# Performance work log

Measured on AMD Instinct MI355X. Metric: run time of the kernel, lower is better.

Reference implementation:

```python
import jax, jax.numpy as jnp
import numpy as np
from jax import lax

B, N, CIN, COUT, FPS, K, TCH, M, H = 8, 4096, 128, 256, 1024, 24, 256, 32, 4
HD = TCH // H
BN_SCALE = 1.0 / np.sqrt(1.0 + 1e-5)  # eval-mode BN: running_mean=0, running_var=1


def _gather(points, idx):
    # points [B,N,C], idx [B,S] or [B,S,K] -> gathered points
    return jax.vmap(lambda p, i: p[i])(points, idx)


def _bn(x, g, b):
    return x * (g * BN_SCALE) + b


def _ln(x, g, b):
    mu = jnp.mean(x, -1, keepdims=True)
    v = jnp.var(x, -1, keepdims=True)
    return (x - mu) / jnp.sqrt(v + 1e-5) * g + b


def _gelu(x):
    return jax.nn.gelu(x, approximate=False)


def _fps(xyz, npoint, farthest0):
    Bb, Nn, _ = xyz.shape
    def step(carry, _):
        dmin, far = carry
        c = jax.vmap(lambda p, i: p[i])(xyz, far)  # [B,3]
        d = jnp.sum((xyz - c[:, None, :]) ** 2, -1)
        dmin = jnp.minimum(dmin, d)
        return (dmin, jnp.argmax(dmin, -1)), far
    init = (jnp.full((Bb, Nn), 1e10, xyz.dtype), farthest0)
    _, cents = lax.scan(step, init, None, length=npoint)
    return cents.T  # [B, npoint]


def _sqdist(src, dst):
    d = -2.0 * jnp.einsum('bnc,bmc->bnm', src, dst)
    d = d + jnp.sum(src ** 2, -1)[:, :, None]
    d = d + jnp.sum(dst ** 2, -1)[:, None, :]
    return d


def _forward(xyz, x, t, farthest0, Wproj, gproj, bproj, Wl1, gl1, bl1, Wl2, gl2, bl2,
             Wc1, gc1, bc1, Wc2, gc2, bc2, Wq, Wk, Wv, Wo,
             ln1g, ln1b, Wqkv, Wao, ln2g, ln2b, Wf1, Wf2):
    # --- GenerateGraph: FPS + KNN grouping ---
    fps_idx = _fps(xyz, FPS, farthest0)            # [B,S]
    new_xyz = _gather(xyz, fps_idx)                # [B,S,3]
    xT = jnp.transpose(x, (0, 2, 1))               # [B,N,Cin]
    new_pts = _gather(xT, fps_idx)                 # [B,S,Cin]
    dist = _sqdist(new_xyz, xyz)                   # [B,S,N]
    _, idx = lax.top_k(-dist, K)                   # [B,S,K] nearest neighbors
    grouped = _gather(xT, idx)                     # [B,S,K,Cin]
    edge = grouped - new_pts[:, :, None, :]
    # --- Local: Conv1DBR proj + Conv1DBRRes (channels-last, 1x1 convs = GEMM) ---
    h = _gelu(_bn(jnp.einsum('bskc,oc->bsko', edge, Wproj), gproj, bproj))
    r = _gelu(_bn(jnp.einsum('bsko,po->bskp', h, Wl1), gl1, bl1))
    r = _bn(jnp.einsum('bskp,op->bsko', r, Wl2), gl2, bl2)
    h = _gelu(r + h)
    f = jnp.max(h, axis=2)                         # adaptive_max_pool over k -> [B,S,O]
    # --- Channel (ca): Conv1DBRRes on centroid features ---
    r = _gelu(_bn(f @ Wc1.T, gc1, bc1))
    r = _bn(r @ Wc2.T, gc2, bc2)
    f = _gelu(r + f)
    x_out = jnp.transpose(f, (0, 2, 1))            # [B,O,S]
    # --- Local2Former: tokens attend to local features ---
    q = t @ Wq.T
    kk = f @ Wk.T
    v = f @ Wv.T
    a = jax.nn.softmax(jnp.einsum('bmd,bsd->bms', q, kk) * (TCH ** -0.5), axis=-1)
    t = t + jnp.einsum('bms,bsd->bmd', a, v) @ Wo.T
    # --- Former: one pre-norm encoder layer (MHA + MLP) ---
    hn = _ln(t, ln1g, ln1b)
    qkv = (hn @ Wqkv.T).reshape(B, M, 3, H, HD).transpose(2, 0, 3, 1, 4)
    qh, kh, vh = qkv[0], qkv[1], qkv[2]            # [B,H,M,hd]
    attn = jax.nn.softmax(jnp.einsum('bhmd,bhnd->bhmn', qh, kh) * (HD ** -0.5), axis=-1)
    o = jnp.einsum('bhmn,bhnd->bhmd', attn, vh).transpose(0, 2, 1, 3).reshape(B, M, TCH)
    t = t + o @ Wao.T
    hn = _ln(t, ln2g, ln2b)
    t = t + _gelu(hn @ Wf1.T) @ Wf2.T
    return new_xyz, x_out, t


def setup_inputs() -> dict:
    key = jax.random.key(0)
    ks = jax.random.split(key, 40)
    def w(k, o, i):
        return jax.random.normal(k, (o, i), jnp.float32) / np.sqrt(i)
    def g(k, c):
        return 1.0 + 0.1 * jax.random.normal(k, (c,), jnp.float32)
    def bta(k, c):
        return 0.1 * jax.random.normal(k, (c,), jnp.float32)
    inp = {
        'xyz': jax.random.normal(ks[0], (B, N, 3), jnp.float32),
        'x': jax.random.normal(ks[1], (B, CIN, N), jnp.float32),
        't': jax.random.normal(ks[2], (B, M, TCH), jnp.float32),
        'farthest0': jax.random.randint(ks[3], (B,), 0, N),
        'Wproj': w(ks[4], COUT, CIN), 'gproj': g(ks[5], COUT), 'bproj': bta(ks[6], COUT),
        'Wl1': w(ks[7], COUT, COUT), 'gl1': g(ks[8], COUT), 'bl1': bta(ks[9], COUT),
        'Wl2': w(ks[10], COUT, COUT), 'gl2': g(ks[11], COUT), 'bl2': bta(ks[12], COUT),
        'Wc1': w(ks[13], COUT, COUT), 'gc1': g(ks[14], COUT), 'bc1': bta(ks[15], COUT),
        'Wc2': w(ks[16], COUT, COUT), 'gc2': g(ks[17], COUT), 'bc2': bta(ks[18], COUT),
        'Wq': w(ks[19], TCH, TCH), 'Wk': w(ks[20], TCH, COUT), 'Wv': w(ks[21], TCH, COUT),
        'Wo': w(ks[22], TCH, TCH),
        'ln1g': g(ks[23], TCH), 'ln1b': bta(ks[24], TCH),
        'Wqkv': w(ks[25], 3 * TCH, TCH), 'Wao': w(ks[26], TCH, TCH),
        'ln2g': g(ks[27], TCH), 'ln2b': bta(ks[28], TCH),
        'Wf1': w(ks[29], 2 * TCH, TCH), 'Wf2': w(ks[30], TCH, 2 * TCH),
    }
    return inp


def reference(xyz, x, t, farthest0, Wproj, gproj, bproj, Wl1, gl1, bl1, Wl2, gl2, bl2,
              Wc1, gc1, bc1, Wc2, gc2, bc2, Wq, Wk, Wv, Wo,
              ln1g, ln1b, Wqkv, Wao, ln2g, ln2b, Wf1, Wf2):
    return _forward(xyz, x, t, farthest0, Wproj, gproj, bproj, Wl1, gl1, bl1, Wl2, gl2, bl2,
                    Wc1, gc1, bc1, Wc2, gc2, bc2, Wq, Wk, Wv, Wo,
                    ln1g, ln1b, Wqkv, Wao, ln2g, ln2b, Wf1, Wf2)
```

## Files before the change

### kernel.cpp

```cpp
#include <hip/hip_runtime.h>
#include <math.h>

#define Bc 8
#define Nc 4096
#define CINc 128
#define COUTc 256
#define Sc 1024
#define Kc 24
#define TCHc 256
#define Mc 32
#define Hc 4
#define HDc 64
#define MBAT (Sc*Kc)

#define BN_SCALE_F 0.9999950000374997f

typedef __attribute__((ext_vector_type(8))) short bf16x8;
typedef __attribute__((ext_vector_type(4))) float f32x4;

__device__ __forceinline__ float b2f(short s){
  unsigned int u = ((unsigned int)(unsigned short)s) << 16;
  union { unsigned int u; float f; } c; c.u = u; return c.f;
}
__device__ __forceinline__ short f2b(float f){
  union { unsigned int u; float f; } c; c.f = f;
  unsigned int u = c.u;
  unsigned int r = (u + 0x7fffu + ((u >> 16) & 1u)) >> 16;
  return (short)(r & 0xffffu);
}
__device__ __forceinline__ float gelu_f(float v){
  return 0.5f * v * (1.f + erff(v * 0.7071067811865475f));
}
__device__ __forceinline__ float rdval(const float* p){ return *p; }
__device__ __forceinline__ float rdval(const short* p){ return b2f(*p); }
__device__ __forceinline__ void wrval(float* p, float v){ *p = v; }
__device__ __forceinline__ void wrval(short* p, float v){ *p = f2b(v); }

__device__ __forceinline__ void gl_lds16(const short* g, short* l){
  __builtin_amdgcn_global_load_lds(
     (const __attribute__((address_space(1))) void*)g,
     (__attribute__((address_space(3))) void*)l, 16, 0, 0);
}

__device__ __forceinline__ void bar_lds(){
  asm volatile("s_waitcnt lgkmcnt(0)" ::: "memory");
  __builtin_amdgcn_s_barrier();
}

template<int CTRL>
__device__ __forceinline__ double dpp_max_f64(double v){
  long long x = __double_as_longlong(v);
  int lo = (int)(unsigned int)(x & 0xFFFFFFFFLL);
  int hi = (int)(unsigned int)((unsigned long long)x >> 32);
  int plo = __builtin_amdgcn_update_dpp(lo, lo, CTRL, 0xF, 0xF, false);
  int phi = __builtin_amdgcn_update_dpp(hi, hi, CTRL, 0xF, 0xF, false);
  double p = __longlong_as_double((long long)(((unsigned long long)(unsigned int)phi << 32)
                                              | (unsigned int)plo));
  return fmax(v, p);
}
template<int CTRL>
__device__ __forceinline__ float dpp_min_f32(float v){
  int x = __float_as_int(v);
  int p = __builtin_amdgcn_update_dpp(x, x, CTRL, 0xF, 0xF, false);
  return fminf(v, __int_as_float(p));
}
template<int CTRL>
__device__ __forceinline__ float dpp_max_f32(float v){
  int x = __float_as_int(v);
  int p = __builtin_amdgcn_update_dpp(x, x, CTRL, 0xF, 0xF, false);
  return fmaxf(v, __int_as_float(p));
}
template<int CTRL>
__device__ __forceinline__ unsigned dpp_min_u32(unsigned v){
  int p = __builtin_amdgcn_update_dpp((int)v, (int)v, CTRL, 0xF, 0xF, false);
  unsigned pu = (unsigned)p;
  return v < pu ? v : pu;
}
__device__ __forceinline__ float wave_min63(float v){
  v = dpp_min_f32<0x111>(v); v = dpp_min_f32<0x112>(v); v = dpp_min_f32<0x114>(v);
  v = dpp_min_f32<0x118>(v); v = dpp_min_f32<0x142>(v); v = dpp_min_f32<0x143>(v);
  return v;
}
__device__ __forceinline__ float wave_max63(float v){
  v = dpp_max_f32<0x111>(v); v = dpp_max_f32<0x112>(v); v = dpp_max_f32<0x114>(v);
  v = dpp_max_f32<0x118>(v); v = dpp_max_f32<0x142>(v); v = dpp_max_f32<0x143>(v);
  return v;
}
__device__ __forceinline__ float bcast63(float v){
  return __int_as_float(__builtin_amdgcn_readlane(__float_as_int(v), 63));
}

#define PREP_FPS 8
#define PREP_TOTAL 256
#define NWORK 248

__global__ __launch_bounds__(512) void prep_kernel(
    const float* __restrict__ xyz, const int* __restrict__ far0, int* __restrict__ fps_idx,
    const float* __restrict__ x, short* __restrict__ xT,
    const float* __restrict__ Wproj, const float* __restrict__ Wl1, const float* __restrict__ Wl2,
    const float* __restrict__ Wc1, const float* __restrict__ Wc2,
    const float* __restrict__ Wk, const float* __restrict__ Wv,
    const float* __restrict__ Wq, const float* __restrict__ Wo,
    const float* __restrict__ Wqkv, const float* __restrict__ Wao,
    const float* __restrict__ Wf1, const float* __restrict__ Wf2,
    const float* __restrict__ t_in,
    short* __restrict__ wbf,
    int* __restrict__ knn_idx, float* __restrict__ out0){
  __shared__ __align__(16) char smemc[57728];
  int bid = blockIdx.x, tid = threadIdx.x;
  if(bid < PREP_FPS){
    int b = bid;
    float* sxyz = (float*)smemc;
    unsigned short* sid = (unsigned short*)(smemc + 49152);
    int* hist = (int*)(smemc + 57344);
    double* pwave = (double*)(smemc + 57600);
    const float* xb = xyz + (size_t)b*Nc*3;
    if(tid < 64) hist[tid] = 0;
    float gx[8], gy[8], gz[8]; int code[8];
    __syncthreads();
#pragma unroll
    for(int j=0;j<8;j++){
      int n = tid + 512*j;
      const float* p = xb + n*3;
      gx[j]=p[0]; gy[j]=p[1]; gz[j]=p[2];
      int qx = (int)fminf(fmaxf((gx[j]+4.2f)*(4.f/8.4f),0.f),3.f);
      int qy = (int)fminf(fmaxf((gy[j]+4.2f)*(4.f/8.4f),0.f),3.f);
      int qz = (int)fminf(fmaxf((gz[j]+4.2f)*(4.f/8.4f),0.f),3.f);
      code[j] = ((qx>>1)<<5)|((qy>>1)<<4)|((qz>>1)<<3)|((qx&1)<<2)|((qy&1)<<1)|(qz&1);
      atomicAdd(&hist[code[j]], 1);
    }
    __syncthreads();
    if(tid==0){
      int run=0;
      for(int i=0;i<64;i++){ int h=hist[i]; hist[i]=run; run+=h; }
    }
    __syncthreads();
#pragma unroll
    for(int j=0;j<8;j++){
      int slot = atomicAdd(&hist[code[j]], 1);
      sxyz[slot*3]=gx[j]; sxyz[slot*3+1]=gy[j]; sxyz[slot*3+2]=gz[j];
      sid[slot] = (unsigned short)(tid + 512*j);
    }
    __syncthreads();
    float px[8], py[8], pz[8], dmin[8];
    unsigned int lokey[8];
    float mnx=3e38f,mny=3e38f,mnz=3e38f,mxx=-3e38f,mxy=-3e38f,mxz=-3e38f;
#pragma unroll
    for(int j=0;j<8;j++){
      int i = (tid>>6)*512 + j*64 + (tid&63);
      float xx=sxyz[i*3], yy=sxyz[i*3+1], zz=sxyz[i*3+2];
      px[j]=xx; py[j]=yy; pz[j]=zz;
      dmin[j]=1e10f;
      lokey[j]=(unsigned int)((Nc-1) - (int)sid[i]);
      mnx=fminf(mnx,xx); mxx=fmaxf(mxx,xx);
      mny=fminf(mny,yy); mxy=fmaxf(mxy,yy);
      mnz=fminf(mnz,zz); mxz=fmaxf(mxz,zz);
    }
    float bbmnx = bcast63(wave_min63(mnx)), bbmxx = bcast63(wave_max63(mxx));
    float bbmny = bcast63(wave_min63(mny)), bbmxy = bcast63(wave_max63(mxy));
    float bbmnz = bcast63(wave_min63(mnz)), bbmxz = bcast63(wave_max63(mxz));
    __syncthreads();
    for(int i=tid; i<Nc; i+=512){
      const float* p = xb + i*3;
      sxyz[i*3]=p[0]; sxyz[i*3+1]=p[1]; sxyz[i*3+2]=p[2];
    }
    __syncthreads();
    int winner = far0[b] & (Nc-1);
    int* out = fps_idx + b*Sc;
    double pk = 0.0;
    float wm = 3.0e38f;
    for(int it=0; it<Sc; it++){
      if(tid==0)
        __hip_atomic_store(&out[it], winner, __ATOMIC_RELAXED, __HIP_MEMORY_SCOPE_AGENT);
      float cx=sxyz[winner*3], cy=sxyz[winner*3+1], cz=sxyz[winner*3+2];
      float ddx = fmaxf(fmaxf(bbmnx - cx, cx - bbmxx), 0.f);
      float ddy = fmaxf(fmaxf(bbmny - cy, cy - bbmxy), 0.f);
      float ddz = fmaxf(fmaxf(bbmnz - cz, cz - bbmxz), 0.f);
      float md2 = ddx*ddx + ddy*ddy + ddz*ddz;
      if(md2 < wm*1.0001f){
        double key[8];
#pragma unroll
        for(int j=0;j<8;j++){
          float dx = __fsub_rn(px[j], cx);
          float dy = __fsub_rn(py[j], cy);
          float dz = __fsub_rn(pz[j], cz);
          float d = __fadd_rn(__fadd_rn(__fmul_rn(dx,dx), __fmul_rn(dy,dy)), __fmul_rn(dz,dz));
          dmin[j] = fminf(dmin[j], d);
          unsigned long long k = (((unsigned long long)__float_as_uint(dmin[j])) << 32) | lokey[j];
          key[j] = __longlong_as_double((long long)k);
        }
#pragma unroll
        for(int st=4; st>0; st>>=1)
#pragma unroll
          for(int j=0;j<st;j++) key[j] = fmax(key[j], key[j+st]);
        double kv = key[0];
        kv = dpp_max_f64<0x111>(kv);
        kv = dpp_max_f64<0x112>(kv);
        kv = dpp_max_f64<0x114>(kv);
        kv = dpp_max_f64<0x118>(kv);
        kv = dpp_max_f64<0x142>(kv);
        kv = dpp_max_f64<0x143>(kv);
        pk = kv;
        wm = __int_as_float(__builtin_amdgcn_readlane(
               (int)(__double_as_longlong(kv) >> 32), 63));
      }
      int p = it & 1;
      if((tid & 63) == 63) pwave[p*8 + (tid>>6)] = pk;
      bar_lds();
      double k0 = pwave[p*8+0], k1 = pwave[p*8+1], k2 = pwave[p*8+2], k3 = pwave[p*8+3];
      double k4 = pwave[p*8+4], k5 = pwave[p*8+5], k6 = pwave[p*8+6], k7 = pwave[p*8+7];
      double kb = fmax(fmax(fmax(k0,k1), fmax(k2,k3)), fmax(fmax(k4,k5), fmax(k6,k7)));
      unsigned long long kbits = (unsigned long long)__double_as_longlong(kb);
      winner = (Nc-1) - (int)(kbits & 0xFFFFFFFFULL);
    }
  } else {
    int wid = bid - PREP_FPS;
    int b = wid / 31;
    int widb = wid % 31;
    short (*tile)[33] = (short(*)[33])smemc;
    for(int t = wid; t < 4096; t += NWORK){
      int bb = t >> 9;
      int rem = t & 511;
      int n0 = (rem & 127) * 32;
      int c0 = (rem >> 7) * 32;
      int tx = tid & 31, ty = tid >> 5;
      __syncthreads();
#pragma unroll
      for(int i=0;i<32;i+=16)
        tile[ty+i][tx] = f2b(x[((size_t)bb*CINc + (c0+ty+i))*Nc + n0+tx]);
      __syncthreads();
#pragma unroll
      for(int i=0;i<32;i+=16)
        xT[((size_t)bb*Nc + (n0+ty+i))*CINc + c0+tx] = tile[tx][ty+i];
    }
    {
      int gid = wid*512 + tid;
      const int stride = NWORK*512;
      short* p = wbf;
      for(int i=gid; i<COUTc*CINc; i+=stride) p[i] = f2b(Wproj[i]);
      p += COUTc*CINc;
      for(int i=gid; i<COUTc*COUTc; i+=stride) p[i] = f2b(Wl1[i]);
      p += COUTc*COUTc;
      for(int i=gid; i<COUTc*COUTc; i+=stride) p[i] = f2b(Wl2[i]);
      p += COUTc*COUTc;
      for(int i=gid; i<COUTc*COUTc; i+=stride) p[i] = f2b(Wc1[i]);
      p += COUTc*COUTc;
      for(int i=gid; i<COUTc*COUTc; i+=stride) p[i] = f2b(Wc2[i]);
      p += COUTc*COUTc;
      for(int i=gid; i<TCHc*COUTc; i+=stride) p[i] = f2b(Wk[i]);
      p += TCHc*COUTc;
      for(int i=gid; i<TCHc*COUTc; i+=stride) p[i] = f2b(Wv[i]);
      p += TCHc*COUTc;
      for(int i=gid; i<TCHc*TCHc; i+=stride) p[i] = f2b(Wq[i]);
      p += TCHc*TCHc;
      for(int i=gid; i<TCHc*TCHc; i+=stride) p[i] = f2b(Wo[i]);
      p += TCHc*TCHc;
      for(int i=gid; i<3*TCHc*TCHc; i+=stride) p[i] = f2b(Wqkv[i]);
      p += 3*TCHc*TCHc;
      for(int i=gid; i<TCHc*TCHc; i+=stride) p[i] = f2b(Wao[i]);
      p += TCHc*TCHc;
      for(int i=gid; i<2*TCHc*TCHc; i+=stride) p[i] = f2b(Wf1[i]);
      p += 2*TCHc*TCHc;
      for(int i=gid; i<2*TCHc*TCHc; i+=stride) p[i] = f2b(Wf2[i]);
      p += 2*TCHc*TCHc;
      for(int i=gid; i<Bc*Mc*TCHc; i+=stride) p[i] = f2b(t_in[i]);
    }
    int* s_qn = (int*)smemc;
    float* pv = (float*)(smemc + 32);
    int*   pi = (int*)(smemc + 64);
    const float* xb = xyz + (size_t)b*Nc*3;
    float px[8], py[8], pz[8], db[8];
#pragma unroll
    for(int j=0;j<8;j++){
      int n = tid + 512*j;
      float xx=xb[n*3], yy=xb[n*3+1], zz=xb[n*3+2];
      px[j]=xx; py[j]=yy; pz[j]=zz;
      db[j] = __fadd_rn(__fadd_rn(__fmul_rn(xx,xx),__fmul_rn(yy,yy)),__fmul_rn(zz,zz));
    }
    __syncthreads();
    for(int s = widb; s < Sc; s += 31){
      if(tid==0){
        int qn;
        for(;;){
          qn = __hip_atomic_load(&fps_idx[b*Sc + s], __ATOMIC_RELAXED, __HIP_MEMORY_SCOPE_AGENT);
          if(qn >= 0) break;
          __builtin_amdgcn_s_sleep(8);
        }
        s_qn[0] = qn & (Nc-1);
      }
      bar_lds();
      int qn = s_qn[0];
      const float* q = xyz + ((size_t)b*Nc + qn)*3;
      float sxq = q[0], syq = q[1], szq = q[2];
      if(tid < 3) out0[((size_t)b*Sc + s)*3 + tid] = q[tid];
      float ss = __fadd_rn(__fadd_rn(__fmul_rn(sxq,sxq),__fmul_rn(syq,syq)),__fmul_rn(szq,szq));
      float dv[8];
#pragma unroll
      for(int j=0;j<8;j++){
        float e = __fmul_rn(sxq,px[j]);
        e = __fadd_rn(e, __fmul_rn(syq,py[j]));
        e = __fadd_rn(e, __fmul_rn(szq,pz[j]));
        dv[j] = __fadd_rn(__fadd_rn(__fmul_rn(-2.f,e), ss), db[j]);
      }
      int* ob = knn_idx + ((size_t)b*Sc + s)*Kc;
      for(int k=0;k<Kc;k++){
        float bvv = dv[0];
#pragma unroll
        for(int j=1;j<8;j++) bvv = fminf(bvv, dv[j]);
        bvv = dpp_min_f32<0x111>(bvv);
        bvv = dpp_min_f32<0x112>(bvv);
        bvv = dpp_min_f32<0x114>(bvv);
        bvv = dpp_min_f32<0x118>(bvv);
        bvv = dpp_min_f32<0x142>(bvv);
        bvv = dpp_min_f32<0x143>(bvv);
        if((tid&63)==63) pv[tid>>6] = bvv;
        bar_lds();
        float vmin = fminf(fminf(fminf(pv[0],pv[1]), fminf(pv[2],pv[3])),
                           fminf(fminf(pv[4],pv[5]), fminf(pv[6],pv[7])));
        unsigned bi = 0xFFFFFFFFu;
#pragma unroll
        for(int j=0;j<8;j++){
          unsigned n = (unsigned)(tid + 512*j);
          if(dv[j]==vmin && n < bi) bi = n;
        }
        bi = dpp_min_u32<0x111>(bi);
        bi = dpp_min_u32<0x112>(bi);
        bi = dpp_min_u32<0x114>(bi);
        bi = dpp_min_u32<0x118>(bi);
        bi = dpp_min_u32<0x142>(bi);
        bi = dpp_min_u32<0x143>(bi);
        if((tid&63)==63) pi[tid>>6] = (int)bi;
        bar_lds();
        unsigned win = (unsigned)pi[0];
#pragma unroll
        for(int w=1;w<8;w++){ unsigned u=(unsigned)pi[w]; win = u<win?u:win; }
        if(tid==0) ob[k] = (int)(win & (Nc-1));
#pragma unroll
        for(int j=0;j<8;j++) if((int)win == tid + 512*j) dv[j] = 3.4e38f;
      }
    }
  }
}

__global__ __launch_bounds__(256) void local_fused(
    const short* __restrict__ xT, const int* __restrict__ knn_idx, const int* __restrict__ fps_idx,
    const short* __restrict__ Wp_, const float* __restrict__ gp, const float* __restrict__ bp,
    const short* __restrict__ W1, const float* __restrict__ g1, const float* __restrict__ b1,
    const short* __restrict__ W2, const float* __restrict__ g2, const float* __restrict__ b2,
    short* __restrict__ Fout){
  __shared__ __align__(16) char lds[77824];
  short* Asrc = (short*)lds;
  short* Wst  = (short*)(lds + 12288);
  short* Hb   = (short*)(lds + 28672);
  short* Rb   = (short*)(lds + 53248);
  int p = blockIdx.x;
  int R0 = p*48;
  int tid = threadIdx.x;
  int w = tid >> 6, lane = tid & 63, quad = lane >> 4, l16 = lane & 15;
  int colbase = w*64;
#pragma unroll
  for(int u0=0; u0<3; u0++){
    int u = tid + u0*256;
    int r = u >> 4, seg = u & 15;
    int Rg = R0 + r;
    int bb = Rg / MBAT;
    int nk = knn_idx[Rg] & (Nc-1);
    int nc = fps_idx[Rg / Kc] & (Nc-1);
    bf16x8 vk = *(const bf16x8*)(xT + ((size_t)bb*Nc + nk)*CINc + seg*8);
    bf16x8 vc = *(const bf16x8*)(xT + ((size_t)bb*Nc + nc)*CINc + seg*8);
    bf16x8 e;
#pragma unroll
    for(int i=0;i<8;i++) e[i] = f2b(__fsub_rn(b2f(vk[i]), b2f(vc[i])));
    *(bf16x8*)&Asrc[((seg>>2)*48 + r)*32 + (seg&3)*8] = e;
  }
  __syncthreads();
  f32x4 acc[3][4];
#pragma unroll
  for(int mt=0;mt<3;mt++)
#pragma unroll
    for(int nt=0;nt<4;nt++) acc[mt][nt] = (f32x4){0.f,0.f,0.f,0.f};
  for(int k0=0; k0<CINc; k0+=32){
#pragma unroll
    for(int c=0;c<4;c++)
      gl_lds16(Wp_ + (size_t)(c*64 + (tid>>2))*CINc + k0 + (tid&3)*8,
               Wst + c*2048 + tid*8);
    __syncthreads();
    bf16x8 af[3], bfr[4];
#pragma unroll
    for(int mt=0;mt<3;mt++) af[mt] = *(const bf16x8*)&Asrc[(((k0>>5))*48 + mt*16 + l16)*32 + quad*8];
#pragma unroll
    for(int nt=0;nt<4;nt++) bfr[nt] = *(const bf16x8*)&Wst[(colbase + nt*16 + l16)*32 + quad*8];
#pragma unroll
    for(int mt=0;mt<3;mt++)
#pragma unroll
      for(int nt=0;nt<4;nt++)
        acc[mt][nt] = __builtin_amdgcn_mfma_f32_16x16x32_bf16(af[mt], bfr[nt], acc[mt][nt], 0, 0, 0);
    __syncthreads();
  }
#pragma unroll
  for(int nt=0;nt<4;nt++){
    int col = colbase + nt*16 + l16;
    float gs = gp[col] * BN_SCALE_F, bs_ = bp[col];
    int kb = col >> 5, kr = col & 31;
#pragma unroll
    for(int mt=0;mt<3;mt++)
#pragma unroll
      for(int r2=0;r2<4;r2++){
        int row = mt*16 + quad*4 + r2;
        float v = acc[mt][nt][r2]*gs + bs_;
        Hb[(kb*48 + row)*32 + kr] = f2b(gelu_f(v));
      }
  }
  __syncthreads();
#pragma unroll
  for(int mt=0;mt<3;mt++)
#pragma unroll
    for(int nt=0;nt<4;nt++) acc[mt][nt] = (f32x4){0.f,0.f,0.f,0.f};
  for(int k0=0; k0<COUTc; k0+=32){
#pragma unroll
    for(int c=0;c<4;c++)
      gl_lds16(W1 + (size_t)(c*64 + (tid>>2))*COUTc + k0 + (tid&3)*8,
               Wst + c*2048 + tid*8);
    __syncthreads();
    bf16x8 af[3], bfr[4];
#pragma unroll
    for(int mt=0;mt<3;mt++) af[mt] = *(const bf16x8*)&Hb[(((k0>>5))*48 + mt*16 + l16)*32 + quad*8];
#pragma unroll
    for(int nt=0;nt<4;nt++) bfr[nt] = *(const bf16x8*)&Wst[(colbase + nt*16 + l16)*32 + quad*8];
#pragma unroll
    for(int mt=0;mt<3;mt++)
#pragma unroll
      for(int nt=0;nt<4;nt++)
        acc[mt][nt] = __builtin_amdgcn_mfma_f32_16x16x32_bf16(af[mt], bfr[nt], acc[mt][nt], 0, 0, 0);
    __syncthreads();
  }
#pragma unroll
  for(int nt=0;nt<4;nt++){
    int col = colbase + nt*16 + l16;
    float gs = g1[col] * BN_SCALE_F, bs_ = b1[col];
    int kb = col >> 5, kr = col & 31;
#pragma unroll
    for(int mt=0;mt<3;mt++)
#pragma unroll
      for(int r2=0;r2<4;r2++){
        int row = mt*16 + quad*4 + r2;
        float v = acc[mt][nt][r2]*gs + bs_;
        Rb[(kb*48 + row)*32 + kr] = f2b(gelu_f(v));
      }
  }
  __syncthreads();
#pragma unroll
  for(int mt=0;mt<3;mt++)
#pragma unroll
    for(int nt=0;nt<4;nt++) acc[mt][nt] = (f32x4){0.f,0.f,0.f,0.f};
  for(int k0=0; k0<COUTc; k0+=32){
#pragma unroll
    for(int c=0;c<4;c++)
      gl_lds16(W2 + (size_t)(c*64 + (tid>>2))*COUTc + k0 + (tid&3)*8,
               Wst + c*2048 + tid*8);
    __syncthreads();
    bf16x8 af[3], bfr[4];
#pragma unroll
    for(int mt=0;mt<3;mt++) af[mt] = *(const bf16x8*)&Rb[(((k0>>5))*48 + mt*16 + l16)*32 + quad*8];
#pragma unroll
    for(int nt=0;nt<4;nt++) bfr[nt] = *(const bf16x8*)&Wst[(colbase + nt*16 + l16)*32 + quad*8];
#pragma unroll
    for(int mt=0;mt<3;mt++)
#pragma unroll
      for(int nt=0;nt<4;nt++)
        acc[mt][nt] = __builtin_amdgcn_mfma_f32_16x16x32_bf16(af[mt], bfr[nt], acc[mt][nt], 0, 0, 0);
    __syncthreads();
  }
#pragma unroll
  for(int nt=0;nt<4;nt++){
    int col = colbase + nt*16 + l16;
    float gs = g2[col] * BN_SCALE_F, bs_ = b2[col];
    int kb = col >> 5, kr = col & 31;
    float gm0 = -3.4e38f, gm1 = -3.4e38f;
#pragma unroll
    for(int mt=0;mt<3;mt++)
#pragma unroll
      for(int r2=0;r2<4;r2++){
        int row = mt*16 + quad*4 + r2;
        float v = acc[mt][nt][r2]*gs + bs_;
        v += b2f(Hb[(kb*48 + row)*32 + kr]);
        v = gelu_f(v);
        if(mt==0) gm0 = fmaxf(gm0, v);
        else if(mt==2) gm1 = fmaxf(gm1, v);
        else { if(quad < 2) gm0 = fmaxf(gm0, v); else gm1 = fmaxf(gm1, v); }
      }
    gm0 = fmaxf(gm0, __shfl_xor(gm0, 16));
    gm0 = fmaxf(gm0, __shfl_xor(gm0, 32));
    gm1 = fmaxf(gm1, __shfl_xor(gm1, 16));
    gm1 = fmaxf(gm1, __shfl_xor(gm1, 32));
    if(quad == 0){
      Fout[(size_t)(p*2)*COUTc + col]     = f2b(gm0);
      Fout[(size_t)(p*2+1)*COUTc + col]   = f2b(gm1);
    }
  }
}

template<int HAS_BN, int HAS_GELU, int HAS_RES, typename TRES, typename TOUT>
__global__ __launch_bounds__(256) void gemm64d(
    const short* __restrict__ A, const short* __restrict__ W,
    const float* __restrict__ g, const float* __restrict__ bias,
    const TRES* __restrict__ Res, TOUT* __restrict__ Out,
    int Nn, int Kk){
  __shared__ short As[64*32];
  __shared__ short Bs[64*32];
  int bm = blockIdx.y*64, bn = blockIdx.x*64;
  int tid = threadIdx.x;
  int wave = tid >> 6, lane = tid & 63, quad = lane >> 4, l16 = lane & 15;
  f32x4 acc[4];
#pragma unroll
  for(int i=0;i<4;i++) acc[i] = (f32x4){0.f,0.f,0.f,0.f};
  const short* Ap = A + (size_t)(bm + (tid>>2))*Kk + (tid&3)*8;
  const short* Wp = W + (size_t)(bn + (tid>>2))*Kk + (tid&3)*8;
  for(int k0=0; k0<Kk; k0+=32){
    gl_lds16(Ap + k0, As + tid*8);
    gl_lds16(Wp + k0, Bs + tid*8);
    __syncthreads();
    bf16x8 a = *(const bf16x8*)&As[(wave*16 + l16)*32 + quad*8];
#pragma unroll
    for(int ct=0; ct<4; ct++){
      bf16x8 bb = *(const bf16x8*)&Bs[(ct*16 + l16)*32 + quad*8];
      acc[ct] = __builtin_amdgcn_mfma_f32_16x16x32_bf16(a, bb, acc[ct], 0, 0, 0);
    }
    __syncthreads();
  }
#pragma unroll
  for(int ct=0; ct<4; ct++){
    int col = bn + ct*16 + l16;
    float gs = 0.f, bs_ = 0.f;
    if(HAS_BN){ gs = g[col] * BN_SCALE_F; bs_ = bias[col]; }
#pragma unroll
    for(int r2=0;r2<4;r2++){
      int row = bm + wave*16 + quad*4 + r2;
      float v = acc[ct][r2];
      if(HAS_BN) v = v*gs + bs_;
      if(HAS_RES) v += rdval(Res + (size_t)row*Nn + col);
      if(HAS_GELU) v = gelu_f(v);
      wrval(Out + (size_t)row*Nn + col, v);
    }
  }
}

__global__ __launch_bounds__(256) void transpose_f(const short* __restrict__ f2, float* __restrict__ out1){
  __shared__ short tile[32][33];
  int b = blockIdx.z;
  int s0 = blockIdx.x*32, c0 = blockIdx.y*32;
  int tx = threadIdx.x & 31, ty = threadIdx.x >> 5;
#pragma unroll
  for(int i=0;i<32;i+=8)
    tile[ty+i][tx] = f2[((size_t)b*Sc + (s0+ty+i))*COUTc + c0+tx];
  __syncthreads();
#pragma unroll
  for(int i=0;i<32;i+=8)
    out1[((size_t)b*COUTc + (c0+ty+i))*Sc + s0+tx] = b2f(tile[tx][ty+i]);
}

__global__ __launch_bounds__(256) void l2f_attn(
    const short* __restrict__ qb, const short* __restrict__ kv,
    short* __restrict__ ao){
  int blk = blockIdx.x; int b = blk / Mc; int m = blk % Mc;
  int tid = threadIdx.x;
  __shared__ float qs[TCHc];
  __shared__ float aw[Sc];
  __shared__ float red[8];
  qs[tid] = b2f(qb[(size_t)(b*Mc+m)*TCHc + tid]);
  __syncthreads();
  float sc[4];
#pragma unroll
  for(int jj=0;jj<4;jj++){
    int j = tid + 256*jj;
    const short* kp = kv + ((size_t)b*Sc + j)*512;
    float a = 0.f;
    for(int c=0;c<TCHc;c+=8){
      bf16x8 v8 = *(const bf16x8*)(kp + c);
#pragma unroll
      for(int i=0;i<8;i++) a += b2f(v8[i]) * qs[c+i];
    }
    sc[jj] = a * 0.0625f;
  }
  float mx = fmaxf(fmaxf(sc[0],sc[1]), fmaxf(sc[2],sc[3]));
#pragma unroll
  for(int off=32; off>0; off>>=1) mx = fmaxf(mx, __shfl_xor(mx, off));
  if((tid&63)==0) red[tid>>6] = mx;
  __syncthreads();
  mx = fmaxf(fmaxf(red[0],red[1]), fmaxf(red[2],red[3]));
  float se = 0.f;
#pragma unroll
  for(int jj=0;jj<4;jj++){
    float e = expf(sc[jj] - mx);
    aw[tid + 256*jj] = e;
    se += e;
  }
#pragma unroll
  for(int off=32; off>0; off>>=1) se += __shfl_xor(se, off);
  if((tid&63)==0) red[4 + (tid>>6)] = se;
  __syncthreads();
  se = red[4]+red[5]+red[6]+red[7];
  float inv = 1.f/se;
#pragma unroll
  for(int jj=0;jj<4;jj++) aw[tid + 256*jj] *= inv;
  __syncthreads();
  float acc = 0.f;
  const short* vp = kv + (size_t)b*Sc*512 + 256 + tid;
  for(int j=0;j<Sc;j++) acc += aw[j] * b2f(vp[(size_t)j*512]);
  ao[(size_t)(b*Mc+m)*TCHc + tid] = f2b(acc);
}

__global__ __launch_bounds__(64) void former_attn(const short* __restrict__ qkv, short* __restrict__ oa){
  int blk = blockIdx.x;
  int m = blk % Mc; int bh = blk / Mc; int h = bh % Hc; int b = bh / Hc;
  int lane = threadIdx.x;
  __shared__ float qs[HDc];
  __shared__ float aw2[32];
  const short* base = qkv + (size_t)(b*Mc)*(3*TCHc);
  qs[lane] = b2f(base[(size_t)m*3*TCHc + h*HDc + lane]);
  __syncthreads();
  int j = lane & 31;
  const short* kp = base + (size_t)j*3*TCHc + TCHc + h*HDc;
  float s = 0.f;
  for(int d=0; d<HDc; d+=8){
    bf16x8 v8 = *(const bf16x8*)(kp + d);
#pragma unroll
    for(int i=0;i<8;i++) s += b2f(v8[i]) * qs[d+i];
  }
  s *= 0.125f;
  float mx = s;
#pragma unroll
  for(int off=16; off>0; off>>=1) mx = fmaxf(mx, __shfl_xor(mx, off, 32));
  float e = expf(s - mx);
  float se = e;
#pragma unroll
  for(int off=16; off>0; off>>=1) se += __shfl_xor(se, off, 32);
  if(lane < 32) aw2[lane] = e / se;
  __syncthreads();
  float acc = 0.f;
  const short* vp = base + 2*TCHc + h*HDc + lane;
  for(int jj=0; jj<32; jj++) acc += aw2[jj] * b2f(vp[(size_t)jj*3*TCHc]);
  oa[(size_t)(b*Mc+m)*TCHc + h*HDc + lane] = f2b(acc);
}

__global__ __launch_bounds__(64) void ln_kernel(const float* __restrict__ X, const float* __restrict__ g,
                                                const float* __restrict__ bb, short* __restrict__ O){
  int row = blockIdx.x, lane = threadIdx.x;
  const float* xp = X + (size_t)row*TCHc;
  float x[4];
#pragma unroll
  for(int j2=0;j2<4;j2++) x[j2] = xp[lane + 64*j2];
  float sm = x[0]+x[1]+x[2]+x[3];
#pragma unroll
  for(int off=32; off>0; off>>=1) sm += __shfl_xor(sm, off);
  float mu = sm * (1.f/256.f);
  float vs = 0.f;
#pragma unroll
  for(int j2=0;j2<4;j2++){ float d = x[j2]-mu; vs += d*d; }
#pragma unroll
  for(int off=32; off>0; off>>=1) vs += __shfl_xor(vs, off);
  float var = vs * (1.f/256.f);
  float rstd = 1.f / sqrtf(var + 1e-5f);
#pragma unroll
  for(int j2=0;j2<4;j2++){
    int c = lane + 64*j2;
    float o = (x[j2]-mu)*rstd*g[c] + bb[c];
    O[(size_t)row*TCHc + c] = f2b(o);
  }
}

extern "C" void kernel_launch(void* const* d_in, const int* in_sizes, int n_in,
                              void* d_out, int out_size, void* d_ws, size_t ws_size,
                              hipStream_t stream){
  const float* xyz  = (const float*)d_in[0];
  const float* x    = (const float*)d_in[1];
  const float* t_in = (const float*)d_in[2];
  const int*   far0 = (const int*)d_in[3];
  const float* Wproj=(const float*)d_in[4];  const float* gproj=(const float*)d_in[5];  const float* bproj=(const float*)d_in[6];
  const float* Wl1 = (const float*)d_in[7];  const float* gl1 = (const float*)d_in[8];  const float* bl1 = (const float*)d_in[9];
  const float* Wl2 = (const float*)d_in[10]; const float* gl2 = (const float*)d_in[11]; const float* bl2 = (const float*)d_in[12];
  const float* Wc1 = (const float*)d_in[13]; const float* gc1 = (const float*)d_in[14]; const float* bc1 = (const float*)d_in[15];
  const float* Wc2 = (const float*)d_in[16]; const float* gc2 = (const float*)d_in[17]; const float* bc2 = (const float*)d_in[18];
  const float* Wq  = (const float*)d_in[19]; const float* Wk  = (const float*)d_in[20]; const float* Wv  = (const float*)d_in[21];
  const float* Wo  = (const float*)d_in[22];
  const float* ln1g= (const float*)d_in[23]; const float* ln1b= (const float*)d_in[24];
  const float* Wqkv= (const float*)d_in[25]; const float* Wao = (const float*)d_in[26];
  const float* ln2g= (const float*)d_in[27]; const float* ln2b= (const float*)d_in[28];
  const float* Wf1 = (const float*)d_in[29]; const float* Wf2 = (const float*)d_in[30];

  char* wsb = (char*)d_ws;
  size_t off = 0;
  auto alloc = [&](size_t bytes)->void*{ void* p = wsb + off; off += (bytes + 255) & ~(size_t)255; return p; };
  int*   fps_i = (int*)alloc((size_t)Bc*Sc*4);
  int*   knn   = (int*)alloc((size_t)Bc*Sc*Kc*4);
  short* xT    = (short*)alloc((size_t)Bc*Nc*CINc*2);
  size_t wbf_elems = (size_t)COUTc*CINc + 4*(size_t)COUTc*COUTc + 2*(size_t)TCHc*COUTc
                   + 2*(size_t)TCHc*TCHc + 3*(size_t)TCHc*TCHc + (size_t)TCHc*TCHc
                   + 2*(size_t)TCHc*TCHc + 2*(size_t)TCHc*TCHc + (size_t)Bc*Mc*TCHc;
  short* wbf   = (short*)alloc(wbf_elems*2);
  short* fbuf  = (short*)alloc((size_t)Bc*Sc*COUTc*2);
  short* rcbuf = (short*)alloc((size_t)Bc*Sc*COUTc*2);
  short* f2buf = (short*)alloc((size_t)Bc*Sc*COUTc*2);
  short* kvbuf = (short*)alloc((size_t)Bc*Sc*512*2);
  short* qbuf  = (short*)alloc((size_t)Bc*Mc*TCHc*2);
  short* a1out = (short*)alloc((size_t)Bc*Mc*TCHc*2);
  float* t1buf = (float*)alloc((size_t)Bc*Mc*TCHc*4);
  short* hnbuf = (short*)alloc((size_t)Bc*Mc*TCHc*2);
  short* qkvb  = (short*)alloc((size_t)Bc*Mc*3*TCHc*2);
  short* a2out = (short*)alloc((size_t)Bc*Mc*TCHc*2);
  float* t2buf = (float*)alloc((size_t)Bc*Mc*TCHc*4);
  short* hn2buf= (short*)alloc((size_t)Bc*Mc*TCHc*2);
  short* g1buf = (short*)alloc((size_t)Bc*Mc*2*TCHc*2);
  if(off > ws_size) return;

  short* wproj_bf = wbf;
  short* wl1_bf   = wproj_bf + COUTc*CINc;
  short* wl2_bf   = wl1_bf + COUTc*COUTc;
  short* wc1_bf   = wl2_bf + COUTc*COUTc;
  short* wc2_bf   = wc1_bf + COUTc*COUTc;
  short* wkv_bf   = wc2_bf + COUTc*COUTc;
  short* wq_bf    = wkv_bf + 2*TCHc*COUTc;
  short* wo_bf    = wq_bf + TCHc*TCHc;
  short* wqkv_bf  = wo_bf + TCHc*TCHc;
  short* wao_bf   = wqkv_bf + 3*TCHc*TCHc;
  short* wf1_bf   = wao_bf + TCHc*TCHc;
  short* wf2_bf   = wf1_bf + 2*TCHc*TCHc;
  short* tbf      = wf2_bf + 2*TCHc*TCHc;

  float* out0 = (float*)d_out;
  float* out1 = out0 + (size_t)Bc*Sc*3;
  float* out2 = out1 + (size_t)Bc*COUTc*Sc;

  hipMemsetAsync(fps_i, 0xFF, (size_t)Bc*Sc*4, stream);
  prep_kernel<<<PREP_TOTAL, 512, 0, stream>>>(xyz, far0, fps_i, x, xT,
                                              Wproj, Wl1, Wl2, Wc1, Wc2, Wk, Wv,
                                              Wq, Wo, Wqkv, Wao, Wf1, Wf2, t_in,
                                              wbf, knn, out0);
  local_fused<<<(Bc*Sc)/2, 256, 0, stream>>>(xT, knn, fps_i,
                                             wproj_bf, gproj, bproj,
                                             wl1_bf, gl1, bl1,
                                             wl2_bf, gl2, bl2, fbuf);
  gemm64d<1,1,0,short,short><<<dim3(COUTc/64, (Bc*Sc)/64), 256, 0, stream>>>(fbuf, wc1_bf, gc1, bc1, (const short*)nullptr, rcbuf, COUTc, COUTc);
  gemm64d<1,1,1,short,short><<<dim3(COUTc/64, (Bc*Sc)/64), 256, 0, stream>>>(rcbuf, wc2_bf, gc2, bc2, fbuf, f2buf, COUTc, COUTc);
  transpose_f<<<dim3(Sc/32, COUTc/32, Bc), 256, 0, stream>>>(f2buf, out1);
  gemm64d<0,0,0,short,short><<<dim3(TCHc/64, (Bc*Mc)/64), 256, 0, stream>>>(tbf, wq_bf, nullptr, nullptr, (const short*)nullptr, qbuf, TCHc, TCHc);
  gemm64d<0,0,0,short,short><<<dim3(512/64, (Bc*Sc)/64), 256, 0, stream>>>(f2buf, wkv_bf, nullptr, nullptr, (const short*)nullptr, kvbuf, 512, COUTc);
  l2f_attn<<<Bc*Mc, 256, 0, stream>>>(qbuf, kvbuf, a1out);
  gemm64d<0,0,1,float,float><<<dim3(TCHc/64, (Bc*Mc)/64), 256, 0, stream>>>(a1out, wo_bf, nullptr, nullptr, t_in, t1buf, TCHc, TCHc);
  ln_kernel<<<Bc*Mc, 64, 0, stream>>>(t1buf, ln1g, ln1b, hnbuf);
  gemm64d<0,0,0,short,short><<<dim3((3*TCHc)/64, (Bc*Mc)/64), 256, 0, stream>>>(hnbuf, wqkv_bf, nullptr, nullptr, (const short*)nullptr, qkvb, 3*TCHc, TCHc);
  former_attn<<<Bc*Hc*Mc, 64, 0, stream>>>(qkvb, a2out);
  gemm64d<0,0,1,float,float><<<dim3(TCHc/64, (Bc*Mc)/64), 256, 0, stream>>>(a2out, wao_bf, nullptr, nullptr, t1buf, t2buf, TCHc, TCHc);
  ln_kernel<<<Bc*Mc, 64, 0, stream>>>(t2buf, ln2g, ln2b, hn2buf);
  gemm64d<0,1,0,short,short><<<dim3((2*TCHc)/64, (Bc*Mc)/64), 256, 0, stream>>>(hn2buf, wf1_bf, nullptr, nullptr, (const short*)nullptr, g1buf, 2*TCHc, TCHc);
  gemm64d<0,0,1,float,float><<<dim3(TCHc/64, (Bc*Mc)/64), 256, 0, stream>>>(g1buf, wf2_bf, nullptr, nullptr, t2buf, out2, TCHc, 2*TCHc);
}
```

Baseline: 1.100 ms.

## Fuse local MLP grouping into KNN worker blocks of prep kernel

Removes the separate local_fused kernel. Each KNN worker block in prep_kernel now runs the edge-feature gather and the three-layer proj/res MLP with max-pool for every query point right after selecting its 24 neighbours, so the local stage overlaps with the FPS dependency wait. A grid-wide ready counter makes the workers wait until all of them have finished the bf16 weight conversion. The cost is that only 248 blocks do all of the MLP work with small 32-row tiles (24 rows used, rows padded with zeros), and the 2x32-column per-wave tiles reuse the weights less than the old 48-row tiles did.

```diff
diff --git a/kernel.cpp b/kernel.cpp
--- a/kernel.cpp
+++ b/kernel.cpp
@@ -46,6 +46,10 @@
   asm volatile("s_waitcnt lgkmcnt(0)" ::: "memory");
   __builtin_amdgcn_s_barrier();
 }
+__device__ __forceinline__ void bar_vm(){
+  asm volatile("s_waitcnt vmcnt(0) lgkmcnt(0)" ::: "memory");
+  __builtin_amdgcn_s_barrier();
+}
 
 template<int CTRL>
 __device__ __forceinline__ double dpp_max_f64(double v){
@@ -105,7 +109,11 @@
     const float* __restrict__ Wf1, const float* __restrict__ Wf2,
     const float* __restrict__ t_in,
     short* __restrict__ wbf,
-    int* __restrict__ knn_idx, float* __restrict__ out0){
+    int* __restrict__ knn_idx, float* __restrict__ out0,
+    const float* __restrict__ gp, const float* __restrict__ bp,
+    const float* __restrict__ g1, const float* __restrict__ b1,
+    const float* __restrict__ g2, const float* __restrict__ b2,
+    short* __restrict__ Fout, int* __restrict__ ready){
   __shared__ __align__(16) char smemc[57728];
   int bid = blockIdx.x, tid = threadIdx.x;
   if(bid < PREP_FPS){
@@ -265,9 +273,24 @@
       p += 2*TCHc*TCHc;
       for(int i=gid; i<Bc*Mc*TCHc; i+=stride) p[i] = f2b(t_in[i]);
     }
+    __syncthreads();
+    if(tid==0){
+      __hip_atomic_fetch_add(ready, 1, __ATOMIC_RELEASE, __HIP_MEMORY_SCOPE_AGENT);
+      while(__hip_atomic_load(ready, __ATOMIC_ACQUIRE, __HIP_MEMORY_SCOPE_AGENT) < NWORK)
+        __builtin_amdgcn_s_sleep(16);
+    }
+    __syncthreads();
     int* s_qn = (int*)smemc;
     float* pv = (float*)(smemc + 32);
     int*   pi = (int*)(smemc + 64);
+    int*   kn = (int*)(smemc + 96);
+    short* Ea = (short*)(smemc + 256);
+    short* Hs = (short*)(smemc + 8448);
+    short* Rs = (short*)(smemc + 24832);
+    short* Ws = (short*)(smemc + 41216);
+    const short* wpj = wbf;
+    const short* w1p = wpj + COUTc*CINc;
+    const short* w2p = w1p + COUTc*COUTc;
     const float* xb = xyz + (size_t)b*Nc*3;
     float px[8], py[8], pz[8], db[8];
 #pragma unroll
@@ -277,6 +300,7 @@
       px[j]=xx; py[j]=yy; pz[j]=zz;
       db[j] = __fadd_rn(__fadd_rn(__fmul_rn(xx,xx),__fmul_rn(yy,yy)),__fmul_rn(zz,zz));
     }
+    int wv8 = tid>>6, qd = (tid>>4)&3, l16v = tid&15;
     __syncthreads();
     for(int s = widb; s < Sc; s += 31){
       if(tid==0){
@@ -334,168 +358,132 @@
         unsigned win = (unsigned)pi[0];
 #pragma unroll
         for(int w=1;w<8;w++){ unsigned u=(unsigned)pi[w]; win = u<win?u:win; }
-        if(tid==0) ob[k] = (int)(win & (Nc-1));
+        if(tid==0){ ob[k] = (int)(win & (Nc-1)); kn[k] = (int)(win & (Nc-1)); }
 #pragma unroll
         for(int j=0;j<8;j++) if((int)win == tid + 512*j) dv[j] = 3.4e38f;
       }
-    }
-  }
-}
-
-__global__ __launch_bounds__(256) void local_fused(
-    const short* __restrict__ xT, const int* __restrict__ knn_idx, const int* __restrict__ fps_idx,
-    const short* __restrict__ Wp_, const float* __restrict__ gp, const float* __restrict__ bp,
-    const short* __restrict__ W1, const float* __restrict__ g1, const float* __restrict__ b1,
-    const short* __restrict__ W2, const float* __restrict__ g2, const float* __restrict__ b2,
-    short* __restrict__ Fout){
-  __shared__ __align__(16) char lds[77824];
-  short* Asrc = (short*)lds;
-  short* Wst  = (short*)(lds + 12288);
-  short* Hb   = (short*)(lds + 28672);
-  short* Rb   = (short*)(lds + 53248);
-  int p = blockIdx.x;
-  int R0 = p*48;
-  int tid = threadIdx.x;
-  int w = tid >> 6, lane = tid & 63, quad = lane >> 4, l16 = lane & 15;
-  int colbase = w*64;
-#pragma unroll
-  for(int u0=0; u0<3; u0++){
-    int u = tid + u0*256;
-    int r = u >> 4, seg = u & 15;
-    int Rg = R0 + r;
-    int bb = Rg / MBAT;
-    int nk = knn_idx[Rg] & (Nc-1);
-    int nc = fps_idx[Rg / Kc] & (Nc-1);
-    bf16x8 vk = *(const bf16x8*)(xT + ((size_t)bb*Nc + nk)*CINc + seg*8);
-    bf16x8 vc = *(const bf16x8*)(xT + ((size_t)bb*Nc + nc)*CINc + seg*8);
-    bf16x8 e;
-#pragma unroll
-    for(int i=0;i<8;i++) e[i] = f2b(__fsub_rn(b2f(vk[i]), b2f(vc[i])));
-    *(bf16x8*)&Asrc[((seg>>2)*48 + r)*32 + (seg&3)*8] = e;
-  }
-  __syncthreads();
-  f32x4 acc[3][4];
-#pragma unroll
-  for(int mt=0;mt<3;mt++)
-#pragma unroll
-    for(int nt=0;nt<4;nt++) acc[mt][nt] = (f32x4){0.f,0.f,0.f,0.f};
-  for(int k0=0; k0<CINc; k0+=32){
-#pragma unroll
-    for(int c=0;c<4;c++)
-      gl_lds16(Wp_ + (size_t)(c*64 + (tid>>2))*CINc + k0 + (tid&3)*8,
-               Wst + c*2048 + tid*8);
-    __syncthreads();
-    bf16x8 af[3], bfr[4];
-#pragma unroll
-    for(int mt=0;mt<3;mt++) af[mt] = *(const bf16x8*)&Asrc[(((k0>>5))*48 + mt*16 + l16)*32 + quad*8];
-#pragma unroll
-    for(int nt=0;nt<4;nt++) bfr[nt] = *(const bf16x8*)&Wst[(colbase + nt*16 + l16)*32 + quad*8];
-#pragma unroll
-    for(int mt=0;mt<3;mt++)
-#pragma unroll
-      for(int nt=0;nt<4;nt++)
-        acc[mt][nt] = __builtin_amdgcn_mfma_f32_16x16x32_bf16(af[mt], bfr[nt], acc[mt][nt], 0, 0, 0);
-    __syncthreads();
-  }
-#pragma unroll
-  for(int nt=0;nt<4;nt++){
-    int col = colbase + nt*16 + l16;
-    float gs = gp[col] * BN_SCALE_F, bs_ = bp[col];
-    int kb = col >> 5, kr = col & 31;
-#pragma unroll
-    for(int mt=0;mt<3;mt++)
-#pragma unroll
-      for(int r2=0;r2<4;r2++){
-        int row = mt*16 + quad*4 + r2;
-        float v = acc[mt][nt][r2]*gs + bs_;
-        Hb[(kb*48 + row)*32 + kr] = f2b(gelu_f(v));
-      }
-  }
-  __syncthreads();
-#pragma unroll
-  for(int mt=0;mt<3;mt++)
-#pragma unroll
-    for(int nt=0;nt<4;nt++) acc[mt][nt] = (f32x4){0.f,0.f,0.f,0.f};
-  for(int k0=0; k0<COUTc; k0+=32){
-#pragma unroll
-    for(int c=0;c<4;c++)
-      gl_lds16(W1 + (size_t)(c*64 + (tid>>2))*COUTc + k0 + (tid&3)*8,
-               Wst + c*2048 + tid*8);
-    __syncthreads();
-    bf16x8 af[3], bfr[4];
-#pragma unroll
-    for(int mt=0;mt<3;mt++) af[mt] = *(const bf16x8*)&Hb[(((k0>>5))*48 + mt*16 + l16)*32 + quad*8];
-#pragma unroll
-    for(int nt=0;nt<4;nt++) bfr[nt] = *(const bf16x8*)&Wst[(colbase + nt*16 + l16)*32 + quad*8];
-#pragma unroll
-    for(int mt=0;mt<3;mt++)
-#pragma unroll
-      for(int nt=0;nt<4;nt++)
-        acc[mt][nt] = __builtin_amdgcn_mfma_f32_16x16x32_bf16(af[mt], bfr[nt], acc[mt][nt], 0, 0, 0);
-    __syncthreads();
-  }
-#pragma unroll
-  for(int nt=0;nt<4;nt++){
-    int col = colbase + nt*16 + l16;
-    float gs = g1[col] * BN_SCALE_F, bs_ = b1[col];
-    int kb = col >> 5, kr = col & 31;
-#pragma unroll
-    for(int mt=0;mt<3;mt++)
-#pragma unroll
-      for(int r2=0;r2<4;r2++){
-        int row = mt*16 + quad*4 + r2;
-        float v = acc[mt][nt][r2]*gs + bs_;
-        Rb[(kb*48 + row)*32 + kr] = f2b(gelu_f(v));
-      }
-  }
-  __syncthreads();
-#pragma unroll
-  for(int mt=0;mt<3;mt++)
-#pragma unroll
-    for(int nt=0;nt<4;nt++) acc[mt][nt] = (f32x4){0.f,0.f,0.f,0.f};
-  for(int k0=0; k0<COUTc; k0+=32){
-#pragma unroll
-    for(int c=0;c<4;c++)
-      gl_lds16(W2 + (size_t)(c*64 + (tid>>2))*COUTc + k0 + (tid&3)*8,
-               Wst + c*2048 + tid*8);
-    __syncthreads();
-    bf16x8 af[3], bfr[4];
-#pragma unroll
-    for(int mt=0;mt<3;mt++) af[mt] = *(const bf16x8*)&Rb[(((k0>>5))*48 + mt*16 + l16)*32 + quad*8];
-#pragma unroll
-    for(int nt=0;nt<4;nt++) bfr[nt] = *(const bf16x8*)&Wst[(colbase + nt*16 + l16)*32 + quad*8];
-#pragma unroll
-    for(int mt=0;mt<3;mt++)
-#pragma unroll
-      for(int nt=0;nt<4;nt++)
-        acc[mt][nt] = __builtin_amdgcn_mfma_f32_16x16x32_bf16(af[mt], bfr[nt], acc[mt][nt], 0, 0, 0);
-    __syncthreads();
-  }
-#pragma unroll
-  for(int nt=0;nt<4;nt++){
-    int col = colbase + nt*16 + l16;
-    float gs = g2[col] * BN_SCALE_F, bs_ = b2[col];
-    int kb = col >> 5, kr = col & 31;
-    float gm0 = -3.4e38f, gm1 = -3.4e38f;
-#pragma unroll
-    for(int mt=0;mt<3;mt++)
-#pragma unroll
-      for(int r2=0;r2<4;r2++){
-        int row = mt*16 + quad*4 + r2;
-        float v = acc[mt][nt][r2]*gs + bs_;
-        v += b2f(Hb[(kb*48 + row)*32 + kr]);
-        v = gelu_f(v);
-        if(mt==0) gm0 = fmaxf(gm0, v);
-        else if(mt==2) gm1 = fmaxf(gm1, v);
-        else { if(quad < 2) gm0 = fmaxf(gm0, v); else gm1 = fmaxf(gm1, v); }
-      }
-    gm0 = fmaxf(gm0, __shfl_xor(gm0, 16));
-    gm0 = fmaxf(gm0, __shfl_xor(gm0, 32));
-    gm1 = fmaxf(gm1, __shfl_xor(gm1, 16));
-    gm1 = fmaxf(gm1, __shfl_xor(gm1, 32));
-    if(quad == 0){
-      Fout[(size_t)(p*2)*COUTc + col]     = f2b(gm0);
-      Fout[(size_t)(p*2+1)*COUTc + col]   = f2b(gm1);
+      bar_lds();
+      {
+        int r = tid>>4, seg = tid&15;
+        bf16x8 e = {0,0,0,0,0,0,0,0};
+        if(r < 24){
+          int nk = kn[r];
+          bf16x8 vk = *(const bf16x8*)(xT + ((size_t)b*Nc + nk)*CINc + seg*8);
+          bf16x8 vc = *(const bf16x8*)(xT + ((size_t)b*Nc + qn)*CINc + seg*8);
+#pragma unroll
+          for(int i=0;i<8;i++) e[i] = f2b(__fsub_rn(b2f(vk[i]), b2f(vc[i])));
+        }
+        *(bf16x8*)&Ea[((seg>>2)*32 + r)*32 + (seg&3)*8] = e;
+      }
+      bar_lds();
+      f32x4 a2[2][2];
+#pragma unroll
+      for(int mt=0;mt<2;mt++)
+#pragma unroll
+        for(int nt=0;nt<2;nt++) a2[mt][nt] = (f32x4){0.f,0.f,0.f,0.f};
+      for(int kb=0; kb<4; kb++){
+        int k0 = kb*32;
+        gl_lds16(wpj + (size_t)(tid>>2)*CINc + k0 + (tid&3)*8, Ws + tid*8);
+        gl_lds16(wpj + (size_t)(128+(tid>>2))*CINc + k0 + (tid&3)*8, Ws + 4096 + tid*8);
+        bar_vm();
+        bf16x8 af0 = *(const bf16x8*)&Ea[(kb*32 + l16v)*32 + qd*8];
+        bf16x8 af1 = *(const bf16x8*)&Ea[(kb*32 + 16 + l16v)*32 + qd*8];
+        bf16x8 b0f = *(const bf16x8*)&Ws[(wv8*32 + l16v)*32 + qd*8];
+        bf16x8 b1f = *(const bf16x8*)&Ws[(wv8*32 + 16 + l16v)*32 + qd*8];
+        a2[0][0] = __builtin_amdgcn_mfma_f32_16x16x32_bf16(af0, b0f, a2[0][0], 0,0,0);
+        a2[0][1] = __builtin_amdgcn_mfma_f32_16x16x32_bf16(af0, b1f, a2[0][1], 0,0,0);
+        a2[1][0] = __builtin_amdgcn_mfma_f32_16x16x32_bf16(af1, b0f, a2[1][0], 0,0,0);
+        a2[1][1] = __builtin_amdgcn_mfma_f32_16x16x32_bf16(af1, b1f, a2[1][1], 0,0,0);
+        bar_lds();
+      }
+#pragma unroll
+      for(int nt=0;nt<2;nt++){
+        int col = wv8*32 + nt*16 + l16v;
+        float gs = gp[col]*BN_SCALE_F, bs_ = bp[col];
+#pragma unroll
+        for(int mt=0;mt<2;mt++)
+#pragma unroll
+          for(int r2=0;r2<4;r2++){
+            int row = mt*16 + qd*4 + r2;
+            float v = a2[mt][nt][r2]*gs + bs_;
+            Hs[(wv8*32 + row)*32 + nt*16 + l16v] = f2b(gelu_f(v));
+          }
+      }
+      bar_lds();
+#pragma unroll
+      for(int mt=0;mt<2;mt++)
+#pragma unroll
+        for(int nt=0;nt<2;nt++) a2[mt][nt] = (f32x4){0.f,0.f,0.f,0.f};
+      for(int kb=0; kb<8; kb++){
+        int k0 = kb*32;
+        gl_lds16(w1p + (size_t)(tid>>2)*COUTc + k0 + (tid&3)*8, Ws + tid*8);
+        gl_lds16(w1p + (size_t)(128+(tid>>2))*COUTc + k0 + (tid&3)*8, Ws + 4096 + tid*8);
+        bar_vm();
+        bf16x8 af0 = *(const bf16x8*)&Hs[(kb*32 + l16v)*32 + qd*8];
+        bf16x8 af1 = *(const bf16x8*)&Hs[(kb*32 + 16 + l16v)*32 + qd*8];
+        bf16x8 b0f = *(const bf16x8*)&Ws[(wv8*32 + l16v)*32 + qd*8];
+        bf16x8 b1f = *(const bf16x8*)&Ws[(wv8*32 + 16 + l16v)*32 + qd*8];
+        a2[0][0] = __builtin_amdgcn_mfma_f32_16x16x32_bf16(af0, b0f, a2[0][0], 0,0,0);
+        a2[0][1] = __builtin_amdgcn_mfma_f32_16x16x32_bf16(af0, b1f, a2[0][1], 0,0,0);
+        a2[1][0] = __builtin_amdgcn_mfma_f32_16x16x32_bf16(af1, b0f, a2[1][0], 0,0,0);
+        a2[1][1] = __builtin_amdgcn_mfma_f32_16x16x32_bf16(af1, b1f, a2[1][1], 0,0,0);
+        bar_lds();
+      }
+#pragma unroll
+      for(int nt=0;nt<2;nt++){
+        int col = wv8*32 + nt*16 + l16v;
+        float gs = g1[col]*BN_SCALE_F, bs_ = b1[col];
+#pragma unroll
+        for(int mt=0;mt<2;mt++)
+#pragma unroll
+          for(int r2=0;r2<4;r2++){
+            int row = mt*16 + qd*4 + r2;
+            float v = a2[mt][nt][r2]*gs + bs_;
+            Rs[(wv8*32 + row)*32 + nt*16 + l16v] = f2b(gelu_f(v));
+          }
+      }
+      bar_lds();
+#pragma unroll
+      for(int mt=0;mt<2;mt++)
+#pragma unroll
+        for(int nt=0;nt<2;nt++) a2[mt][nt] = (f32x4){0.f,0.f,0.f,0.f};
+      for(int kb=0; kb<8; kb++){
+        int k0 = kb*32;
+        gl_lds16(w2p + (size_t)(tid>>2)*COUTc + k0 + (tid&3)*8, Ws + tid*8);
+        gl_lds16(w2p + (size_t)(128+(tid>>2))*COUTc + k0 + (tid&3)*8, Ws + 4096 + tid*8);
+        bar_vm();
+        bf16x8 af0 = *(const bf16x8*)&Rs[(kb*32 + l16v)*32 + qd*8];
+        bf16x8 af1 = *(const bf16x8*)&Rs[(kb*32 + 16 + l16v)*32 + qd*8];
+        bf16x8 b0f = *(const bf16x8*)&Ws[(wv8*32 + l16v)*32 + qd*8];
+        bf16x8 b1f = *(const bf16x8*)&Ws[(wv8*32 + 16 + l16v)*32 + qd*8];
+        a2[0][0] = __builtin_amdgcn_mfma_f32_16x16x32_bf16(af0, b0f, a2[0][0], 0,0,0);
+        a2[0][1] = __builtin_amdgcn_mfma_f32_16x16x32_bf16(af0, b1f, a2[0][1], 0,0,0);
+        a2[1][0] = __builtin_amdgcn_mfma_f32_16x16x32_bf16(af1, b0f, a2[1][0], 0,0,0);
+        a2[1][1] = __builtin_amdgcn_mfma_f32_16x16x32_bf16(af1, b1f, a2[1][1], 0,0,0);
+        bar_lds();
+      }
+#pragma unroll
+      for(int nt=0;nt<2;nt++){
+        int col = wv8*32 + nt*16 + l16v;
+        float gs = g2[col]*BN_SCALE_F, bs_ = b2[col];
+        float gm = -3.4e38f;
+#pragma unroll
+        for(int mt=0;mt<2;mt++)
+#pragma unroll
+          for(int r2=0;r2<4;r2++){
+            int row = mt*16 + qd*4 + r2;
+            if(row < 24){
+              float v = a2[mt][nt][r2]*gs + bs_;
+              v += b2f(Hs[(wv8*32 + row)*32 + nt*16 + l16v]);
+              gm = fmaxf(gm, gelu_f(v));
+            }
+          }
+        gm = fmaxf(gm, __shfl_xor(gm, 16));
+        gm = fmaxf(gm, __shfl_xor(gm, 32));
+        if(qd==0)
+          Fout[((size_t)b*Sc + s)*COUTc + col] = f2b(gm);
+      }
+      bar_lds();
     }
   }
 }
@@ -693,6 +681,7 @@
   auto alloc = [&](size_t bytes)->void*{ void* p = wsb + off; off += (bytes + 255) & ~(size_t)255; return p; };
   int*   fps_i = (int*)alloc((size_t)Bc*Sc*4);
   int*   knn   = (int*)alloc((size_t)Bc*Sc*Kc*4);
+  int*   ready = (int*)alloc(256);
   short* xT    = (short*)alloc((size_t)Bc*Nc*CINc*2);
   size_t wbf_elems = (size_t)COUTc*CINc + 4*(size_t)COUTc*COUTc + 2*(size_t)TCHc*COUTc
                    + 2*(size_t)TCHc*TCHc + 3*(size_t)TCHc*TCHc + (size_t)TCHc*TCHc
@@ -732,14 +721,13 @@
   float* out2 = out1 + (size_t)Bc*COUTc*Sc;
 
   hipMemsetAsync(fps_i, 0xFF, (size_t)Bc*Sc*4, stream);
+  hipMemsetAsync(ready, 0, 4, stream);
   prep_kernel<<<PREP_TOTAL, 512, 0, stream>>>(xyz, far0, fps_i, x, xT,
                                               Wproj, Wl1, Wl2, Wc1, Wc2, Wk, Wv,
                                               Wq, Wo, Wqkv, Wao, Wf1, Wf2, t_in,
-                                              wbf, knn, out0);
-  local_fused<<<(Bc*Sc)/2, 256, 0, stream>>>(xT, knn, fps_i,
-                                             wproj_bf, gproj, bproj,
-                                             wl1_bf, gl1, bl1,
-                                             wl2_bf, gl2, bl2, fbuf);
+                                              wbf, knn, out0,
+                                              gproj, bproj, gl1, bl1, gl2, bl2,
+                                              fbuf, ready);
   gemm64d<1,1,0,short,short><<<dim3(COUTc/64, (Bc*Sc)/64), 256, 0, stream>>>(fbuf, wc1_bf, gc1, bc1, (const short*)nullptr, rcbuf, COUTc, COUTc);
   gemm64d<1,1,1,short,short><<<dim3(COUTc/64, (Bc*Sc)/64), 256, 0, stream>>>(rcbuf, wc2_bf, gc2, bc2, fbuf, f2buf, COUTc, COUTc);
   transpose_f<<<dim3(Sc/32, COUTc/32, Bc), 256, 0, stream>>>(f2buf, out1);
```

After: 1.263 ms. 1.15x slower.
